# Kernel optimization log

Measured on AMD Instinct MI355X. Metric: run time of the kernel, lower is better.

The kernel has to match this reference:

```python
import jax, jax.numpy as jnp
import numpy as np
from jax import lax

NT, NB, NC = 128, 256, 512
HID, EMB, NCLS, NSTEPS, POSE = 256, 128, 37, 25, 256
RNN_IN = NC + EMB + POSE + 576  # 1472, matches GRUCell input dim


def roi_align_2x2(feat, boxes):
    # feat: [C,H,W] -- image 0 only, faithful to roi_align(features, [coord], (2,2))
    # which assigns all nB boxes to batch element 0.
    # boxes: [nB,4] = (x1,y1,x2,y2), torchvision semantics (aligned=False,
    # spatial_scale=1); sampling_ratio fixed to 1 (one sample per bin center).
    C, H, W = feat.shape
    x1, y1, x2, y2 = boxes[:, 0], boxes[:, 1], boxes[:, 2], boxes[:, 3]
    bw = jnp.maximum(x2 - x1, 1.0) * 0.5  # bin width  (output 2x2)
    bh = jnp.maximum(y2 - y1, 1.0) * 0.5  # bin height
    off = jnp.array([0.5, 1.5], boxes.dtype)
    ys = y1[:, None] + off[None, :] * bh[:, None]            # [nB,2]
    xs = x1[:, None] + off[None, :] * bw[:, None]            # [nB,2]
    yy = jnp.broadcast_to(ys[:, :, None], ys.shape + (2,))   # [nB,2,2]
    xx = jnp.broadcast_to(xs[:, None, :], xs.shape[:1] + (2, 2))
    valid = (yy >= -1.0) & (yy <= H) & (xx >= -1.0) & (xx <= W)
    y = jnp.clip(yy, 0.0, H - 1.0)
    x = jnp.clip(xx, 0.0, W - 1.0)
    y0 = jnp.floor(y); x0 = jnp.floor(x)
    y0i = y0.astype(jnp.int32); x0i = x0.astype(jnp.int32)
    y1i = jnp.minimum(y0i + 1, H - 1); x1i = jnp.minimum(x0i + 1, W - 1)
    ly = y - y0; lx = x - x0; hy = 1.0 - ly; hx = 1.0 - lx
    g = lambda yi, xi: feat[:, yi, xi]                       # [C,nB,2,2]
    val = (g(y0i, x0i) * (hy * hx) + g(y0i, x1i) * (hy * lx)
           + g(y1i, x0i) * (ly * hx) + g(y1i, x1i) * (ly * lx))
    val = jnp.where(valid[None], val, 0.0)                   # [C,nB,2,2]
    return jnp.transpose(val, (1, 0, 2, 3)).reshape(val.shape[1], -1)  # [nB,4C]


def setup_inputs() -> dict:
    key = jax.random.key(0)
    ks = jax.random.split(key, 20)
    s = 0.05
    return {
        "feats": jax.random.normal(ks[0], (NT, NB, NC), jnp.float32),
        "pose": jax.random.normal(ks[1], (NB, POSE, 1, NT), jnp.float32),
        "pyr0": jax.random.normal(ks[2], (NB, 16, 16, 128), jnp.float32),
        "pyr1": jax.random.normal(ks[3], (NB, 64, 8, 64), jnp.float32),
        "pyr2": jax.random.normal(ks[4], (NB, 64, 4, 65), jnp.float32),
        "text_length": jnp.full((NB,), NSTEPS, jnp.int32),
        "text": jax.random.randint(ks[5], (NB * NSTEPS,), 0, NCLS),
        # parameters
        "i2h_w": jax.random.normal(ks[6], (HID, NC)) * s,
        "h2h_w": jax.random.normal(ks[7], (HID, HID)) * s,
        "h2h_b": jnp.zeros((HID,)),
        "score_w": jax.random.normal(ks[8], (HID,)) * s,
        "pose_w": jax.random.normal(ks[9], (4, NC + POSE)) * s,
        "pose_b": jnp.zeros((4,)),
        "gru_w_ih": jax.random.normal(ks[10], (3 * HID, RNN_IN)) * s,
        "gru_w_hh": jax.random.normal(ks[11], (3 * HID, HID)) * s,
        "gru_b_ih": jnp.zeros((3 * HID,)),
        "gru_b_hh": jnp.zeros((3 * HID,)),
        "char_emb": jax.random.normal(ks[12], (NCLS + 1, EMB)),
        "gen_w": jax.random.normal(ks[13], (NCLS, HID)) * s,
        "gen_b": jnp.zeros((NCLS,)),
    }


def reference(feats, pose, pyr0, pyr1, pyr2, text_length, text,
              i2h_w, h2h_w, h2h_b, score_w, pose_w, pose_b,
              gru_w_ih, gru_w_hh, gru_b_ih, gru_b_hh,
              char_emb, gen_w, gen_b):
    nT, nB, nC = feats.shape
    # pose.squeeze(2).permute(2,0,1) -> [nT,nB,POSE]
    pose_t = jnp.transpose(pose[:, :, 0, :], (2, 0, 1))
    feats_cat = jnp.concatenate([feats, pose_t], axis=2)       # [nT,nB,nC+POSE]
    feats_proj = jnp.einsum('tbc,hc->tbh', feats, i2h_w)       # i2h, no bias

    # targets: <start>=0 then text+1 per sample (equal lengths -> reshape)
    tgt = text.reshape(nB, NSTEPS).astype(jnp.int32) + 1
    targets = jnp.concatenate([jnp.zeros((nB, 1), jnp.int32), tgt], axis=1).T  # [NSTEPS+1,nB]

    pyramid = (pyr0, pyr1, pyr2)

    def step(hidden, tgt_row):
        emb = char_emb[tgt_row]                                # [nB,EMB]
        hp = hidden @ h2h_w.T + h2h_b                          # [nB,HID]
        e = jnp.tanh(feats_proj + hp[None]) @ score_w          # [nT,nB]
        alpha = jax.nn.softmax(e, axis=0)
        ctx = jnp.einsum('tbc,tb->bc', feats_cat, alpha)       # [nB,nC+POSE]
        coord = jax.nn.sigmoid(ctx @ pose_w.T + pose_b)        # [nB,4]
        crops = []
        for f in pyramid:
            h, w = f.shape[2], f.shape[3]
            scale = jnp.array([h, w, h, w], coord.dtype)
            coord = coord * scale                              # faithful in-loop rescale
            crops.append(roi_align_2x2(f[0], coord))           # [nB,4*C_i]
        x = jnp.concatenate([ctx, emb] + crops, axis=1)        # [nB,RNN_IN]
        gi = x @ gru_w_ih.T + gru_b_ih
        gh = hidden @ gru_w_hh.T + gru_b_hh
        ir, iz, inn = jnp.split(gi, 3, axis=1)
        hr, hz, hn = jnp.split(gh, 3, axis=1)
        r = jax.nn.sigmoid(ir + hr)
        z = jax.nn.sigmoid(iz + hz)
        n = jnp.tanh(inn + r * hn)
        h_new = (1.0 - z) * n + z * hidden
        return h_new, h_new

    hidden0 = jnp.zeros((nB, HID), feats.dtype)
    _, hs = lax.scan(step, hidden0, targets[:NSTEPS])          # [NSTEPS,nB,HID]
    # re-pack per-sample (equal lengths): [b0 t0..t24, b1 t0..t24, ...]
    new_h = jnp.transpose(hs, (1, 0, 2)).reshape(nB * NSTEPS, HID)
    probs = new_h @ gen_w.T + gen_b                            # [nB*NSTEPS,NCLS]
    return probs
```

## Files before the change

kernel.cpp:

```cpp
#include <hip/hip_runtime.h>
#include <hip/hip_bf16.h>

typedef unsigned short u16;
typedef unsigned int u32;
typedef __attribute__((ext_vector_type(8))) short short8;
typedef __attribute__((ext_vector_type(4))) float floatx4;

#define NT 128
#define NB 256
#define NC 512
#define HID 256
#define EMB 128
#define NCLS 37
#define NSTEPS 25
#define POSEC 256
#define RNN_IN 1472

__device__ __forceinline__ float b2f(u16 u) {
    union { float f; u32 i; } v; v.i = ((u32)u) << 16; return v.f;
}
__device__ __forceinline__ u16 f2b(float f) {
    union { float f; u32 i; } v; v.f = f;
    u32 x = v.i;
    return (u16)((x + 0x7fffu + ((x >> 16) & 1u)) >> 16);
}
__device__ __forceinline__ float sigm(float x) { return 1.f / (1.f + __expf(-x)); }

__device__ __forceinline__ float ftanh(float x) {
    float t = __expf(-2.f * fabsf(x));
    float r = (1.f - t) * __builtin_amdgcn_rcpf(1.f + t);
    return copysignf(r, x);
}

__device__ __forceinline__ float ldf(const float* p, size_t i) { return p[i]; }
__device__ __forceinline__ float ldf(const u16* p, size_t i) { return b2f(p[i]); }

__device__ __forceinline__ short8 ld8(const u16* p) { return *(const short8*)p; }
__device__ __forceinline__ short8 ld8(const float* p) {
    float4 a = *(const float4*)p; float4 b = *(const float4*)(p + 4);
    short8 r;
    r[0] = (short)f2b(a.x); r[1] = (short)f2b(a.y); r[2] = (short)f2b(a.z); r[3] = (short)f2b(a.w);
    r[4] = (short)f2b(b.x); r[5] = (short)f2b(b.y); r[6] = (short)f2b(b.z); r[7] = (short)f2b(b.w);
    return r;
}
__device__ __forceinline__ float4 ld4(const float* p) { return *(const float4*)p; }
__device__ __forceinline__ float4 ld4(const u16* p) {
    ushort4 v = *(const ushort4*)p;
    return make_float4(b2f(v.x), b2f(v.y), b2f(v.z), b2f(v.w));
}

__global__ void probe_kernel(const void* score_w, int* flag) {
    __shared__ float red[128];
    int tid = threadIdx.x;
    const u16* p = (const u16*)score_w;
    float v = fabsf(b2f(p[tid]));
    v = (v == v && v < 1e6f) ? v : 1e6f;
    red[tid] = v;
    __syncthreads();
    for (int s2 = 64; s2 > 0; s2 >>= 1) {
        if (tid < s2) red[tid] += red[tid + s2];
        __syncthreads();
    }
    if (tid == 0) flag[0] = (red[0] < 1000.f) ? 1 : 0;
}

__global__ void conv_kernel(const void* w_ih, const void* w_hh, const void* h2h_w,
                            u16* out_ih, u16* out_hh, u16* out_h2h, const int* flagp) {
    int f = *flagp;
    int idx = blockIdx.x * blockDim.x + threadIdx.x;
    int stride = gridDim.x * blockDim.x;
    const int n_ih = 768 * RNN_IN, n_hh = 768 * HID, n_h2h = HID * HID;
    if (f) {
        const u16* a = (const u16*)w_ih; const u16* b = (const u16*)w_hh;
        const u16* c = (const u16*)h2h_w;
        for (int i = idx; i < n_ih; i += stride) out_ih[i] = a[i];
        for (int i = idx; i < n_hh; i += stride) out_hh[i] = b[i];
        for (int i = idx; i < n_h2h; i += stride) {
            int j = i >> 8, cc = i & 255;
            out_h2h[(cc >> 1) * 512 + (j << 1) + (cc & 1)] = c[i];
        }
    } else {
        const float* a = (const float*)w_ih; const float* b = (const float*)w_hh;
        const float* c = (const float*)h2h_w;
        for (int i = idx; i < n_ih; i += stride) out_ih[i] = f2b(a[i]);
        for (int i = idx; i < n_hh; i += stride) out_hh[i] = f2b(b[i]);
        for (int i = idx; i < n_h2h; i += stride) {
            int j = i >> 8, cc = i & 255;
            out_h2h[(cc >> 1) * 512 + (j << 1) + (cc & 1)] = f2b(c[i]);
        }
    }
}

template <typename T>
__device__ void pconv_body(const T* pose, u16* pt) {
    size_t n = (size_t)NB * POSEC * NT;
    size_t i = ((size_t)blockIdx.x * blockDim.x + threadIdx.x) * 4;
    size_t stride = (size_t)gridDim.x * blockDim.x * 4;
    for (; i < n; i += stride) {
        float4 v = ld4(pose + i);
        ushort4 o;
        o.x = f2b(v.x); o.y = f2b(v.y); o.z = f2b(v.z); o.w = f2b(v.w);
        *(ushort4*)(pt + i) = o;
    }
}
__global__ __launch_bounds__(256) void pconv_kernel(const void* pose, u16* pt, const int* flagp) {
    if (*flagp) pconv_body((const u16*)pose, pt);
    else        pconv_body((const float*)pose, pt);
}

template <typename T>
__device__ void trans_body(const T* feats, u16* ft) {
    int b = blockIdx.x, t0 = blockIdx.y * 8;
    #pragma unroll
    for (int half = 0; half < 2; half++) {
        int c = threadIdx.x + half * 256;
        short8 v;
        #pragma unroll
        for (int j = 0; j < 8; j++)
            v[j] = (short)f2b(ldf(feats, ((size_t)(t0 + j) * NB + b) * NC + c));
        *(short8*)(ft + ((size_t)b * NC + c) * NT + t0) = v;
    }
}
__global__ __launch_bounds__(256) void trans_kernel(const void* feats, u16* ft, const int* flagp) {
    if (*flagp) trans_body((const u16*)feats, ft);
    else        trans_body((const float*)feats, ft);
}

template <typename T>
__device__ void fp_body(const T* feats, const T* i2h_w, u16* fp) {
    __shared__ u16 As[128][40];
    __shared__ u16 Bs[128][40];
    const int tid = threadIdx.x;
    const int w = tid >> 6, lane = tid & 63;
    const int m0 = blockIdx.x * 128, n0 = blockIdx.y * 128;
    const int lr = lane & 15, kq = (lane >> 4) * 8;
    const int srow = tid >> 1, schunk = (tid & 1) * 16;

    floatx4 acc[2][8];
    #pragma unroll
    for (int i = 0; i < 2; i++)
        #pragma unroll
        for (int nt = 0; nt < 8; nt++) acc[i][nt] = (floatx4){0.f, 0.f, 0.f, 0.f};

    for (int kk = 0; kk < NC; kk += 32) {
        short8 av0 = ld8(feats + (size_t)(m0 + srow) * NC + kk + schunk);
        short8 av1 = ld8(feats + (size_t)(m0 + srow) * NC + kk + schunk + 8);
        short8 bv0 = ld8(i2h_w + (size_t)(n0 + srow) * NC + kk + schunk);
        short8 bv1 = ld8(i2h_w + (size_t)(n0 + srow) * NC + kk + schunk + 8);
        __syncthreads();
        *(short8*)&As[srow][schunk] = av0;
        *(short8*)&As[srow][schunk + 8] = av1;
        *(short8*)&Bs[srow][schunk] = bv0;
        *(short8*)&Bs[srow][schunk + 8] = bv1;
        __syncthreads();
        short8 a0 = *(const short8*)&As[w * 32 + lr][kq];
        short8 a1 = *(const short8*)&As[w * 32 + 16 + lr][kq];
        #pragma unroll
        for (int nt = 0; nt < 8; nt++) {
            short8 bf = *(const short8*)&Bs[nt * 16 + lr][kq];
            acc[0][nt] = __builtin_amdgcn_mfma_f32_16x16x32_bf16(a0, bf, acc[0][nt], 0, 0, 0);
            acc[1][nt] = __builtin_amdgcn_mfma_f32_16x16x32_bf16(a1, bf, acc[1][nt], 0, 0, 0);
        }
    }

    int rbase = (lane >> 4) * 4, col = lane & 15;
    #pragma unroll
    for (int i = 0; i < 2; i++)
        #pragma unroll
        for (int nt = 0; nt < 8; nt++)
            #pragma unroll
            for (int r = 0; r < 4; r++) {
                int m = m0 + w * 32 + i * 16 + rbase + r;
                int t = m >> 8, b = m & 255;
                fp[((size_t)b * NT + t) * HID + n0 + nt * 16 + col] = f2b(acc[i][nt][r]);
            }
}
__global__ __launch_bounds__(256) void fp_kernel(const void* feats, const void* i2h_w,
                                                 u16* fp, const int* flagp) {
    if (*flagp) fp_body((const u16*)feats, (const u16*)i2h_w, fp);
    else        fp_body((const float*)feats, (const float*)i2h_w, fp);
}

template <typename T>
__device__ __forceinline__ void do_crop(
    const T* __restrict__ f, int C, int H, int W,
    float x1, float y1, float x2, float y2,
    u16* __restrict__ xrow, int off, int tid)
{
    int n = C * 4;
    if (tid >= n) return;
    float bw = fmaxf(x2 - x1, 1.f) * 0.5f;
    float bh = fmaxf(y2 - y1, 1.f) * 0.5f;
    int c = tid >> 2, iy = (tid >> 1) & 1, ix = tid & 1;
    float yy = y1 + (0.5f + (float)iy) * bh;
    float xx = x1 + (0.5f + (float)ix) * bw;
    bool valid = (yy >= -1.f) && (yy <= (float)H) && (xx <= (float)W) && (xx >= -1.f);
    float y = fminf(fmaxf(yy, 0.f), (float)(H - 1));
    float x = fminf(fmaxf(xx, 0.f), (float)(W - 1));
    float y0f = floorf(y), x0f = floorf(x);
    int y0 = (int)y0f, x0 = (int)x0f;
    int y1i = min(y0 + 1, H - 1), x1i = min(x0 + 1, W - 1);
    float ly = y - y0f, lx = x - x0f, hy = 1.f - ly, hx = 1.f - lx;
    size_t base = (size_t)c * H * W;
    float v = ldf(f, base + y0 * W + x0) * hy * hx + ldf(f, base + y0 * W + x1i) * hy * lx
            + ldf(f, base + y1i * W + x0) * ly * hx + ldf(f, base + y1i * W + x1i) * ly * lx;
    xrow[off + tid] = f2b(valid ? v : 0.f);
}

template <typename T>
__device__ void attn_body(
    const u16* pt,
    const T* pyr0, const T* pyr1, const T* pyr2,
    const int* text,
    const T* h2h_b, const T* score_w,
    const T* pose_w, const T* pose_b, const T* char_emb,
    const u16* h2h_wT, const u16* ft, const u16* fp,
    const u16* h_cur, u16* xout, int s)
{
    const int b = blockIdx.x;
    const int tid = threadIdx.x;
    __shared__ __align__(16) float smem[2708];
    float* h_s    = smem;
    float* hp_s   = smem + 256;
    float* sw_s   = smem + 520;
    float* ep_s   = smem + 784;
    float* pp_s   = smem + 1296;
    float* e_s    = smem + 1808;
    float* ctx_s  = smem + 1936;
    float* coord_s= smem + 2704;

    float hv = 0.f, swv = 0.f;
    if (tid < 256) hv = b2f(h_cur[b * HID + tid]);
    else           swv = ldf(score_w, tid - 256);

    u32 wv[64];
    {
        const u16* wp = h2h_wT + 2 * (tid & 255) + (size_t)(tid >> 8) * 64 * 512;
        #pragma unroll
        for (int i = 0; i < 64; i++) wv[i] = *(const u32*)(wp + i * 512);
    }

    const int t_e = tid >> 2, q_e = tid & 3;
    const u16* fpr = fp + ((size_t)b * NT + t_e) * HID + q_e * 64;
    short8 fpv[8];
    #pragma unroll
    for (int i = 0; i < 8; i++) fpv[i] = *(const short8*)(fpr + 8 * i);

    const u16* ftr = ft + ((size_t)b * NC + tid) * NT;
    short8 ftv[16];
    #pragma unroll
    for (int i = 0; i < 16; i++) ftv[i] = *(const short8*)(ftr + 8 * i);

    int tgt = 0;
    if (s > 0) tgt = text[b * NSTEPS + (s - 1)] + 1;
    float embv = 0.f;
    if (tid >= 256 && tid < 256 + EMB)
        embv = ldf(char_emb, (size_t)tgt * EMB + (tid - 256));

    if (tid < 256) h_s[tid] = hv;
    else { int k = tid - 256; sw_s[k + (k >> 5)] = swv; }
    __syncthreads();

    {
        int base = (tid >> 8) * 128;
        float acc = 0.f;
        #pragma unroll
        for (int i = 0; i < 64; i++) {
            u32 w2 = wv[i];
            acc += h_s[base + 2 * i] * b2f((u16)w2)
                 + h_s[base + 2 * i + 1] * b2f((u16)(w2 >> 16));
        }
        ep_s[tid] = acc;
    }
    __syncthreads();
    if (tid < 256) hp_s[tid + (tid >> 5)] = ep_s[tid] + ep_s[tid + 256] + ldf(h2h_b, tid);
    __syncthreads();

    {
        float acc = 0.f;
        #pragma unroll
        for (int i = 0; i < 8; i++) {
            short8 v = fpv[i];
            #pragma unroll
            for (int j = 0; j < 8; j++) {
                int h = q_e * 64 + i * 8 + j;
                int ki = h + (h >> 5);
                acc += ftanh(b2f((u16)v[j]) + hp_s[ki]) * sw_s[ki];
            }
        }
        ep_s[tid] = acc;
    }
    __syncthreads();

    if (tid < 64) {
        float4 a = *(const float4*)&ep_s[4 * tid];
        float4 c = *(const float4*)&ep_s[4 * (tid + 64)];
        float eL = a.x + a.y + a.z + a.w;
        float eH = c.x + c.y + c.z + c.w;
        float m = fmaxf(eL, eH);
        #pragma unroll
        for (int off = 32; off; off >>= 1) m = fmaxf(m, __shfl_xor(m, off));
        float pL = __expf(eL - m), pH = __expf(eH - m);
        float sm = pL + pH;
        #pragma unroll
        for (int off = 32; off; off >>= 1) sm += __shfl_xor(sm, off);
        float inv = 1.f / sm;
        e_s[tid] = pL * inv;
        e_s[tid + 64] = pH * inv;
    }
    __syncthreads();

    u16* xr = xout + (size_t)b * RNN_IN;

    {
        float acc = 0.f;
        #pragma unroll
        for (int i = 0; i < 16; i++) {
            float4 a0 = *(const float4*)&e_s[8 * i];
            float4 a1 = *(const float4*)&e_s[8 * i + 4];
            short8 v = ftv[i];
            acc += a0.x * b2f((u16)v[0]) + a0.y * b2f((u16)v[1])
                 + a0.z * b2f((u16)v[2]) + a0.w * b2f((u16)v[3])
                 + a1.x * b2f((u16)v[4]) + a1.y * b2f((u16)v[5])
                 + a1.z * b2f((u16)v[6]) + a1.w * b2f((u16)v[7]);
        }
        ctx_s[tid] = acc;
        xr[tid] = f2b(acc);
    }
    {
        const int p_c = tid & 255, hf = tid >> 8;
        const u16* pr = pt + ((size_t)b * POSEC + p_c) * NT + hf * 64;
        float acc = 0.f;
        #pragma unroll
        for (int i = 0; i < 8; i++) {
            short8 v = *(const short8*)(pr + 8 * i);
            float4 a0 = *(const float4*)&e_s[hf * 64 + 8 * i];
            float4 a1 = *(const float4*)&e_s[hf * 64 + 8 * i + 4];
            acc += a0.x * b2f((u16)v[0]) + a0.y * b2f((u16)v[1])
                 + a0.z * b2f((u16)v[2]) + a0.w * b2f((u16)v[3])
                 + a1.x * b2f((u16)v[4]) + a1.y * b2f((u16)v[5])
                 + a1.z * b2f((u16)v[6]) + a1.w * b2f((u16)v[7]);
        }
        pp_s[tid] = acc;
    }
    if (tid >= 256 && tid < 256 + EMB) xr[768 + (tid - 256)] = f2b(embv);
    __syncthreads();
    if (tid < 256) {
        float v = pp_s[tid] + pp_s[tid + 256];
        ctx_s[512 + tid] = v;
        xr[512 + tid] = f2b(v);
    }
    __syncthreads();

    if (tid < 256) {
        int j = tid >> 6, lane = tid & 63;
        float acc = 0.f;
        #pragma unroll
        for (int k = 0; k < 12; k++)
            acc += ctx_s[lane + k * 64] * ldf(pose_w, (size_t)j * 768 + k * 64 + lane);
        #pragma unroll
        for (int off = 32; off; off >>= 1) acc += __shfl_down(acc, off);
        if (lane == 0) coord_s[j] = sigm(acc + ldf(pose_b, j));
    }
    __syncthreads();

    float c0 = coord_s[0], c1 = coord_s[1], c2 = coord_s[2], c3 = coord_s[3];
    if (tid < 64) {
        do_crop(pyr0, 16, 16, 128, c0 * 16.f,  c1 * 128.f,    c2 * 16.f,  c3 * 128.f,    xr, 896,  tid);
        do_crop(pyr2, 64, 4,  65,  c0 * 512.f, c1 * 532480.f, c2 * 512.f, c3 * 532480.f, xr, 1216, tid + 192);
    } else if (tid < 320) {
        do_crop(pyr1, 64, 8,  64,  c0 * 128.f, c1 * 8192.f,   c2 * 128.f, c3 * 8192.f,   xr, 960,  tid - 64);
    } else {
        do_crop(pyr2, 64, 4,  65,  c0 * 512.f, c1 * 532480.f, c2 * 512.f, c3 * 532480.f, xr, 1216, tid - 320);
    }
}

__global__ __launch_bounds__(512) void attn_kernel(
    const u16* pt,
    const void* pyr0, const void* pyr1, const void* pyr2,
    const int* text,
    const void* h2h_b, const void* score_w,
    const void* pose_w, const void* pose_b, const void* char_emb,
    const u16* h2h_wT, const u16* ft, const u16* fp,
    const u16* h_cur, u16* xout, int s, const int* flagp)
{
    if (*flagp)
        attn_body(pt, (const u16*)pyr0, (const u16*)pyr1,
                  (const u16*)pyr2, text, (const u16*)h2h_b, (const u16*)score_w,
                  (const u16*)pose_w, (const u16*)pose_b, (const u16*)char_emb,
                  h2h_wT, ft, fp, h_cur, xout, s);
    else
        attn_body(pt, (const float*)pyr0, (const float*)pyr1,
                  (const float*)pyr2, text, (const float*)h2h_b, (const float*)score_w,
                  (const float*)pose_w, (const float*)pose_b, (const float*)char_emb,
                  h2h_wT, ft, fp, h_cur, xout, s);
}

template <typename T>
__device__ void gru_body(
    const u16* x, const u16* h_prev, u16* h_new,
    const u16* w_ih, const u16* w_hh, const T* b_ih, const T* b_hh)
{
    const int jt = blockIdx.x, bt = blockIdx.y;
    const int tid = threadIdx.x;
    const int w = tid >> 6, lane = tid & 63;
    const int lr = lane & 15;
    const int kq = (lane >> 4) * 8;
    const int arow = bt * 16 + lr;

    floatx4 acc_r = {0.f,0.f,0.f,0.f}, acc_z = acc_r, acc_in = acc_r, acc_hn = acc_r;

    for (int kc = w; kc < RNN_IN / 32; kc += 8) {
        int k0 = kc * 32 + kq;
        short8 a = *(const short8*)(x + (size_t)arow * RNN_IN + k0);
        short8 b0 = *(const short8*)(w_ih + (size_t)(0 * HID + jt * 16 + lr) * RNN_IN + k0);
        short8 b1 = *(const short8*)(w_ih + (size_t)(1 * HID + jt * 16 + lr) * RNN_IN + k0);
        short8 b2 = *(const short8*)(w_ih + (size_t)(2 * HID + jt * 16 + lr) * RNN_IN + k0);
        acc_r  = __builtin_amdgcn_mfma_f32_16x16x32_bf16(a, b0, acc_r, 0, 0, 0);
        acc_z  = __builtin_amdgcn_mfma_f32_16x16x32_bf16(a, b1, acc_z, 0, 0, 0);
        acc_in = __builtin_amdgcn_mfma_f32_16x16x32_bf16(a, b2, acc_in, 0, 0, 0);
    }
    for (int kc = w; kc < HID / 32; kc += 8) {
        int k0 = kc * 32 + kq;
        short8 a = *(const short8*)(h_prev + (size_t)arow * HID + k0);
        short8 b0 = *(const short8*)(w_hh + (size_t)(0 * HID + jt * 16 + lr) * HID + k0);
        short8 b1 = *(const short8*)(w_hh + (size_t)(1 * HID + jt * 16 + lr) * HID + k0);
        short8 b2 = *(const short8*)(w_hh + (size_t)(2 * HID + jt * 16 + lr) * HID + k0);
        acc_r  = __builtin_amdgcn_mfma_f32_16x16x32_bf16(a, b0, acc_r, 0, 0, 0);
        acc_z  = __builtin_amdgcn_mfma_f32_16x16x32_bf16(a, b1, acc_z, 0, 0, 0);
        acc_hn = __builtin_amdgcn_mfma_f32_16x16x32_bf16(a, b2, acc_hn, 0, 0, 0);
    }

    extern __shared__ float red[];
    int jcol = lane & 15, rb = (lane >> 4) * 4;
    #pragma unroll
    for (int r = 0; r < 4; r++) {
        red[((w * 4 + 0) * 16 + jcol) * 17 + rb + r] = acc_r[r];
        red[((w * 4 + 1) * 16 + jcol) * 17 + rb + r] = acc_z[r];
        red[((w * 4 + 2) * 16 + jcol) * 17 + rb + r] = acc_in[r];
        red[((w * 4 + 3) * 16 + jcol) * 17 + rb + r] = acc_hn[r];
    }
    __syncthreads();

    if (tid < 256) {
        int jj = tid >> 4, bl = tid & 15;
        float sr = 0, sz = 0, sin_ = 0, shn = 0;
        #pragma unroll
        for (int w2 = 0; w2 < 8; w2++) {
            sr   += red[((w2 * 4 + 0) * 16 + jj) * 17 + bl];
            sz   += red[((w2 * 4 + 1) * 16 + jj) * 17 + bl];
            sin_ += red[((w2 * 4 + 2) * 16 + jj) * 17 + bl];
            shn  += red[((w2 * 4 + 3) * 16 + jj) * 17 + bl];
        }
        int j = jt * 16 + jj, b = bt * 16 + bl;
        float r  = sigm(sr + ldf(b_ih, j) + ldf(b_hh, j));
        float zz = sigm(sz + ldf(b_ih, j + 256) + ldf(b_hh, j + 256));
        float n  = ftanh(sin_ + ldf(b_ih, j + 512) + r * (shn + ldf(b_hh, j + 512)));
        float hp = b2f(h_prev[(size_t)b * HID + j]);
        h_new[(size_t)b * HID + j] = f2b((1.f - zz) * n + zz * hp);
    }
}

__global__ __launch_bounds__(512) void gru_kernel(
    const u16* x, const u16* h_prev, u16* h_new,
    const u16* w_ih, const u16* w_hh,
    const void* b_ih, const void* b_hh, const int* flagp)
{
    if (*flagp) gru_body(x, h_prev, h_new, w_ih, w_hh, (const u16*)b_ih, (const u16*)b_hh);
    else        gru_body(x, h_prev, h_new, w_ih, w_hh, (const float*)b_ih, (const float*)b_hh);
}

template <typename T>
__device__ void gen_body(const u16* hs, const T* gen_w, const T* gen_b, void* out) {
    int rowid = blockIdx.x;
    int b = rowid / NSTEPS, s = rowid % NSTEPS;
    const u16* h = hs + ((size_t)(s + 1) * NB + b) * HID;
    extern __shared__ float hsd[];
    int tid = threadIdx.x;
    for (int i = tid; i < HID; i += 64) hsd[i] = b2f(h[i]);
    __syncthreads();
    if (tid < NCLS) {
        float acc = ldf(gen_b, tid);
        const T* wr = gen_w + (size_t)tid * HID;
        #pragma unroll 4
        for (int k4 = 0; k4 < HID / 4; k4++) {
            float4 wv = ld4(wr + 4 * k4);
            acc += hsd[4 * k4 + 0] * wv.x + hsd[4 * k4 + 1] * wv.y
                 + hsd[4 * k4 + 2] * wv.z + hsd[4 * k4 + 3] * wv.w;
        }
        size_t o = (size_t)rowid * NCLS + tid;
        if (sizeof(T) == 2) ((u16*)out)[o] = f2b(acc);
        else                ((float*)out)[o] = acc;
    }
}
__global__ __launch_bounds__(64) void gen_kernel(
    const u16* hs, const void* gen_w, const void* gen_b, void* out, const int* flagp)
{
    if (*flagp) gen_body(hs, (const u16*)gen_w, (const u16*)gen_b, out);
    else        gen_body(hs, (const float*)gen_w, (const float*)gen_b, out);
}

extern "C" void kernel_launch(void* const* d_in, const int* in_sizes, int n_in,
                              void* d_out, int out_size, void* d_ws, size_t ws_size,
                              hipStream_t stream) {
    (void)in_sizes; (void)n_in; (void)out_size;
    const int* text = (const int*)d_in[6];

    char* ws = (char*)d_ws;
    size_t off = 256;
    int* flag = (int*)ws;
    u16* fp = (u16*)(ws + off); off += (size_t)NB * NT * HID * 2;
    u16* ft = (u16*)(ws + off); off += (size_t)NB * NC * NT * 2;
    u16* hs     = (u16*)(ws + off); off += 3407872;
    u16* x      = (u16*)(ws + off); off += 753664;
    u16* wih_c  = (u16*)(ws + off); off += 2260992;
    u16* whh_c  = (u16*)(ws + off); off += 393216;
    u16* h2h_wT = (u16*)(ws + off); off += 131072;
    u16* pt     = (u16*)(ws + off); off += (size_t)NB * POSEC * NT * 2;

    probe_kernel<<<1, 128, 0, stream>>>(d_in[10], flag);
    conv_kernel<<<512, 256, 0, stream>>>(d_in[13], d_in[14], d_in[8],
                                         wih_c, whh_c, h2h_wT, flag);
    hipMemsetAsync(hs, 0, (size_t)NB * HID * 2, stream);
    fp_kernel<<<dim3(256, 2), 256, 0, stream>>>(d_in[0], d_in[7], fp, flag);
    trans_kernel<<<dim3(NB, NT / 8), 256, 0, stream>>>(d_in[0], ft, flag);
    pconv_kernel<<<2048, 256, 0, stream>>>(d_in[1], pt, flag);

    for (int s = 0; s < NSTEPS; s++) {
        attn_kernel<<<NB, 512, 0, stream>>>(
            pt, d_in[2], d_in[3], d_in[4], text,
            d_in[9], d_in[10], d_in[11], d_in[12], d_in[17],
            h2h_wT, ft, fp, hs + (size_t)s * NB * HID, x, s, flag);
        gru_kernel<<<dim3(16, 16), 512, 34816, stream>>>(
            x, hs + (size_t)s * NB * HID, hs + (size_t)(s + 1) * NB * HID,
            wih_c, whh_c, d_in[15], d_in[16], flag);
    }
    gen_kernel<<<NB * NSTEPS, 64, 1024, stream>>>(hs, d_in[18], d_in[19], d_out, flag);
}
```

Before: 1.042 ms.

## Widen fp GEMM tile and prefetch pose data early in attention kernel

The fp projection GEMM now uses 512-thread blocks that each compute the full 256-wide hidden dimension, so the feats tile is loaded once instead of twice and the grid halves. In the attention kernel, the pose-transposed rows and the pose_w/pose_b weights are loaded into registers at kernel start so their latency overlaps the earlier compute. The pose-sum reduction is folded into the coord dot product, which removes one __syncthreads and the ctx_s write of the pose context. The cost is higher register pressure in the attention kernel, which may lower occupancy.

After: 1.037 ms. About the same (-0.5%).

```diff
diff --git a/kernel.cpp b/kernel.cpp
--- a/kernel.cpp
+++ b/kernel.cpp
@@ -129,53 +129,57 @@
 template <typename T>
 __device__ void fp_body(const T* feats, const T* i2h_w, u16* fp) {
     __shared__ u16 As[128][40];
-    __shared__ u16 Bs[128][40];
+    __shared__ u16 Bs[256][40];
     const int tid = threadIdx.x;
     const int w = tid >> 6, lane = tid & 63;
-    const int m0 = blockIdx.x * 128, n0 = blockIdx.y * 128;
+    const int wm = w >> 2, wn = w & 3;
+    const int m0 = blockIdx.x * 128;
     const int lr = lane & 15, kq = (lane >> 4) * 8;
-    const int srow = tid >> 1, schunk = (tid & 1) * 16;
-
-    floatx4 acc[2][8];
-    #pragma unroll
-    for (int i = 0; i < 2; i++)
-        #pragma unroll
-        for (int nt = 0; nt < 8; nt++) acc[i][nt] = (floatx4){0.f, 0.f, 0.f, 0.f};
+    const int arow = tid >> 2, achunk = (tid & 3) * 8;
+    const int brow = tid >> 1, bchunk = (tid & 1) * 16;
+
+    floatx4 acc[4][4];
+    #pragma unroll
+    for (int mt = 0; mt < 4; mt++)
+        #pragma unroll
+        for (int nt = 0; nt < 4; nt++) acc[mt][nt] = (floatx4){0.f, 0.f, 0.f, 0.f};
 
     for (int kk = 0; kk < NC; kk += 32) {
-        short8 av0 = ld8(feats + (size_t)(m0 + srow) * NC + kk + schunk);
-        short8 av1 = ld8(feats + (size_t)(m0 + srow) * NC + kk + schunk + 8);
-        short8 bv0 = ld8(i2h_w + (size_t)(n0 + srow) * NC + kk + schunk);
-        short8 bv1 = ld8(i2h_w + (size_t)(n0 + srow) * NC + kk + schunk + 8);
+        short8 av  = ld8(feats + (size_t)(m0 + arow) * NC + kk + achunk);
+        short8 bv0 = ld8(i2h_w + (size_t)brow * NC + kk + bchunk);
+        short8 bv1 = ld8(i2h_w + (size_t)brow * NC + kk + bchunk + 8);
         __syncthreads();
-        *(short8*)&As[srow][schunk] = av0;
-        *(short8*)&As[srow][schunk + 8] = av1;
-        *(short8*)&Bs[srow][schunk] = bv0;
-        *(short8*)&Bs[srow][schunk + 8] = bv1;
+        *(short8*)&As[arow][achunk] = av;
+        *(short8*)&Bs[brow][bchunk] = bv0;
+        *(short8*)&Bs[brow][bchunk + 8] = bv1;
         __syncthreads();
-        short8 a0 = *(const short8*)&As[w * 32 + lr][kq];
-        short8 a1 = *(const short8*)&As[w * 32 + 16 + lr][kq];
-        #pragma unroll
-        for (int nt = 0; nt < 8; nt++) {
-            short8 bf = *(const short8*)&Bs[nt * 16 + lr][kq];
-            acc[0][nt] = __builtin_amdgcn_mfma_f32_16x16x32_bf16(a0, bf, acc[0][nt], 0, 0, 0);
-            acc[1][nt] = __builtin_amdgcn_mfma_f32_16x16x32_bf16(a1, bf, acc[1][nt], 0, 0, 0);
+        short8 af[4];
+        #pragma unroll
+        for (int mt = 0; mt < 4; mt++)
+            af[mt] = *(const short8*)&As[wm * 64 + mt * 16 + lr][kq];
+        #pragma unroll
+        for (int nt = 0; nt < 4; nt++) {
+            short8 bf = *(const short8*)&Bs[wn * 64 + nt * 16 + lr][kq];
+            #pragma unroll
+            for (int mt = 0; mt < 4; mt++)
+                acc[mt][nt] = __builtin_amdgcn_mfma_f32_16x16x32_bf16(af[mt], bf, acc[mt][nt], 0, 0, 0);
         }
     }
 
     int rbase = (lane >> 4) * 4, col = lane & 15;
     #pragma unroll
-    for (int i = 0; i < 2; i++)
-        #pragma unroll
-        for (int nt = 0; nt < 8; nt++)
+    for (int mt = 0; mt < 4; mt++)
+        #pragma unroll
+        for (int nt = 0; nt < 4; nt++)
             #pragma unroll
             for (int r = 0; r < 4; r++) {
-                int m = m0 + w * 32 + i * 16 + rbase + r;
+                int m = m0 + wm * 64 + mt * 16 + rbase + r;
                 int t = m >> 8, b = m & 255;
-                fp[((size_t)b * NT + t) * HID + n0 + nt * 16 + col] = f2b(acc[i][nt][r]);
+                int h = wn * 64 + nt * 16 + col;
+                fp[((size_t)b * NT + t) * HID + h] = f2b(acc[mt][nt][r]);
             }
 }
-__global__ __launch_bounds__(256) void fp_kernel(const void* feats, const void* i2h_w,
+__global__ __launch_bounds__(512) void fp_kernel(const void* feats, const void* i2h_w,
                                                  u16* fp, const int* flagp) {
     if (*flagp) fp_body((const u16*)feats, (const u16*)i2h_w, fp);
     else        fp_body((const float*)feats, (const float*)i2h_w, fp);
@@ -219,7 +223,7 @@
 {
     const int b = blockIdx.x;
     const int tid = threadIdx.x;
-    __shared__ __align__(16) float smem[2708];
+    __shared__ __align__(16) float smem[2452];
     float* h_s    = smem;
     float* hp_s   = smem + 256;
     float* sw_s   = smem + 520;
@@ -227,7 +231,7 @@
     float* pp_s   = smem + 1296;
     float* e_s    = smem + 1808;
     float* ctx_s  = smem + 1936;
-    float* coord_s= smem + 2704;
+    float* coord_s= smem + 2448;
 
     float hv = 0.f, swv = 0.f;
     if (tid < 256) hv = b2f(h_cur[b * HID + tid]);
@@ -250,6 +254,21 @@
     short8 ftv[16];
     #pragma unroll
     for (int i = 0; i < 16; i++) ftv[i] = *(const short8*)(ftr + 8 * i);
+
+    const int p_c = tid & 255, hf = tid >> 8;
+    const u16* ptr_ = pt + ((size_t)b * POSEC + p_c) * NT + hf * 64;
+    short8 ptv[8];
+    #pragma unroll
+    for (int i = 0; i < 8; i++) ptv[i] = *(const short8*)(ptr_ + 8 * i);
+
+    float pwv[12];
+    {
+        int j = (tid >> 6) & 3, lane = tid & 63;
+        #pragma unroll
+        for (int k = 0; k < 12; k++)
+            pwv[k] = (tid < 256) ? ldf(pose_w, (size_t)j * 768 + k * 64 + lane) : 0.f;
+    }
+    float pbv = (tid < 256 && (tid & 63) == 0) ? ldf(pose_b, tid >> 6) : 0.f;
 
     int tgt = 0;
     if (s > 0) tgt = text[b * NSTEPS + (s - 1)] + 1;
@@ -328,12 +347,10 @@
         xr[tid] = f2b(acc);
     }
     {
-        const int p_c = tid & 255, hf = tid >> 8;
-        const u16* pr = pt + ((size_t)b * POSEC + p_c) * NT + hf * 64;
         float acc = 0.f;
         #pragma unroll
         for (int i = 0; i < 8; i++) {
-            short8 v = *(const short8*)(pr + 8 * i);
+            short8 v = ptv[i];
             float4 a0 = *(const float4*)&e_s[hf * 64 + 8 * i];
             float4 a1 = *(const float4*)&e_s[hf * 64 + 8 * i + 4];
             acc += a0.x * b2f((u16)v[0]) + a0.y * b2f((u16)v[1])
@@ -345,22 +362,24 @@
     }
     if (tid >= 256 && tid < 256 + EMB) xr[768 + (tid - 256)] = f2b(embv);
     __syncthreads();
+
     if (tid < 256) {
-        float v = pp_s[tid] + pp_s[tid + 256];
-        ctx_s[512 + tid] = v;
-        xr[512 + tid] = f2b(v);
-    }
-    __syncthreads();
-
-    if (tid < 256) {
-        int j = tid >> 6, lane = tid & 63;
+        int lane = tid & 63;
         float acc = 0.f;
         #pragma unroll
-        for (int k = 0; k < 12; k++)
-            acc += ctx_s[lane + k * 64] * ldf(pose_w, (size_t)j * 768 + k * 64 + lane);
+        for (int k = 0; k < 8; k++)
+            acc += ctx_s[lane + k * 64] * pwv[k];
+        #pragma unroll
+        for (int k = 8; k < 12; k++) {
+            int p = lane + (k - 8) * 64;
+            acc += (pp_s[p] + pp_s[p + 256]) * pwv[k];
+        }
         #pragma unroll
         for (int off = 32; off; off >>= 1) acc += __shfl_down(acc, off);
-        if (lane == 0) coord_s[j] = sigm(acc + ldf(pose_b, j));
+        if (lane == 0) coord_s[tid >> 6] = sigm(acc + pbv);
+    } else {
+        int p = tid - 256;
+        xr[512 + p] = f2b(pp_s[p] + pp_s[p + 256]);
     }
     __syncthreads();
 
@@ -522,7 +541,7 @@
     conv_kernel<<<512, 256, 0, stream>>>(d_in[13], d_in[14], d_in[8],
                                          wih_c, whh_c, h2h_wT, flag);
     hipMemsetAsync(hs, 0, (size_t)NB * HID * 2, stream);
-    fp_kernel<<<dim3(256, 2), 256, 0, stream>>>(d_in[0], d_in[7], fp, flag);
+    fp_kernel<<<256, 512, 0, stream>>>(d_in[0], d_in[7], fp, flag);
     trans_kernel<<<dim3(NB, NT / 8), 256, 0, stream>>>(d_in[0], ft, flag);
     pconv_kernel<<<2048, 256, 0, stream>>>(d_in[1], pt, flag);
 
```
